# Kernel tuning notes

Hardware: AMD Instinct MI355X
Metric: run time of the kernel (lower is better)

## Reference

```python
import jax, jax.numpy as jnp
import numpy as np

T, B, D, H = 256, 64, 1024, 1024


def setup_inputs() -> dict:
    key = jax.random.key(0)
    ks = jax.random.split(key, 7)
    s = 1.0 / np.sqrt(H)
    return {
        "x": jax.random.normal(ks[0], (T, B, D), dtype=jnp.float32),
        "h0": jax.random.normal(ks[1], (B, H), dtype=jnp.float32),
        "c0": jax.random.normal(ks[2], (B, H), dtype=jnp.float32),
        "W_ih": jax.random.normal(ks[3], (4 * H, D), dtype=jnp.float32) * s,
        "W_hh": jax.random.normal(ks[4], (4 * H, H), dtype=jnp.float32) * s,
        "b_ih": jax.random.normal(ks[5], (4 * H,), dtype=jnp.float32) * s,
        "b_hh": jax.random.normal(ks[6], (4 * H,), dtype=jnp.float32) * s,
    }


def reference(x, h0, c0, W_ih, W_hh, b_ih, b_hh):
    # Reversed-time LSTM: process t = T-1 .. 0, outputs stored in original order.
    def step(carry, xt):
        h, c = carry
        gates = xt @ W_ih.T + b_ih + h @ W_hh.T + b_hh  # [B, 4H]
        i, f, g, o = jnp.split(gates, 4, axis=-1)
        c = jax.nn.sigmoid(f) * c + jax.nn.sigmoid(i) * jnp.tanh(g)
        h = jax.nn.sigmoid(o) * jnp.tanh(c)
        return (h, c), h

    (hT, cT), ys = jax.lax.scan(step, (h0, c0), x, reverse=True)
    return ys, hT, cT
```

## Files before the change

kernel.cpp:

```cpp
#include <hip/hip_runtime.h>
#include <stdint.h>
#include <stddef.h>


typedef unsigned short u16;
typedef __attribute__((ext_vector_type(4))) unsigned short u16x4;
typedef __attribute__((ext_vector_type(8))) short short8;
typedef __attribute__((ext_vector_type(4))) float f32x4;

#define T_LEN 256
#define YS_ELEMS (256 * 64 * 1024)

__device__ __forceinline__ u16 f2bf(float f) {
  union { float f; unsigned int i; } v; v.f = f;
  unsigned int r = v.i + 0x7FFFu + ((v.i >> 16) & 1u);
  return (u16)(r >> 16);
}
__device__ __forceinline__ float bf2f(u16 u) {
  union { unsigned int i; float f; } v; v.i = ((unsigned int)u) << 16; return v.f;
}
__device__ __forceinline__ void gload_lds16(const void* g, void* l) {
  __builtin_amdgcn_global_load_lds(
      (const __attribute__((address_space(1))) unsigned int*)g,
      (__attribute__((address_space(3))) unsigned int*)l, 16, 0, 0);
}
__device__ __forceinline__ float sigm_fast(float x) { return 1.f / (1.f + __expf(-x)); }

#define ISSUE_LD16C(dst, ptr, off)                                      \
  asm volatile("global_load_dwordx4 %0, %1, off offset:%c2"             \
               : "=v"(dst) : "v"(ptr), "i"(off) : "memory")

#define LD8_PLAIN(dst, ptr)                                             \
  asm volatile("global_load_dwordx2 %0, %1, off"                        \
               : "=v"(dst) : "v"(ptr) : "memory")

#define ST8_WT(ptr, val)                                                \
  asm volatile("global_store_dwordx2 %0, %1, off sc0 sc1"               \
               :: "v"(ptr), "v"(val) : "memory")

#define WAIT_VM16() do { asm volatile("s_waitcnt vmcnt(16)" ::: "memory"); \
                         __builtin_amdgcn_sched_barrier(0); } while (0)
#define WAIT_VM0()  do { asm volatile("s_waitcnt vmcnt(0)"  ::: "memory"); \
                         __builtin_amdgcn_sched_barrier(0); } while (0)

__global__ void cast_f32_bf16(const float* __restrict__ src, u16* __restrict__ dst, int n4) {
  int i = blockIdx.x * blockDim.x + threadIdx.x;
  const int stride = gridDim.x * blockDim.x;
  for (; i < n4; i += stride) {
    float4 v = ((const float4*)src)[i];
    u16x4 o;
    o[0] = f2bf(v.x); o[1] = f2bf(v.y); o[2] = f2bf(v.z); o[3] = f2bf(v.w);
    ((u16x4*)dst)[i] = o;
  }
}

__global__ void scat_h0(const float* __restrict__ src, u16* __restrict__ dst) {
  int i = blockIdx.x * blockDim.x + threadIdx.x;
  const int b = i >> 7;
  const int j0 = (i & 127) * 8;
  const float4 v0 = ((const float4*)src)[i * 2];
  const float4 v1 = ((const float4*)src)[i * 2 + 1];
  short8 pk;
  pk[0] = (short)f2bf(v0.x); pk[1] = (short)f2bf(v0.y);
  pk[2] = (short)f2bf(v0.z); pk[3] = (short)f2bf(v0.w);
  pk[4] = (short)f2bf(v1.x); pk[5] = (short)f2bf(v1.y);
  pk[6] = (short)f2bf(v1.z); pk[7] = (short)f2bf(v1.w);
  *(short8*)(dst + (size_t)(j0 >> 4) * 1024 + b * 16 + (j0 & 15)) = pk;
}

__global__ void canary_k(float* __restrict__ out) { out[0] = 100.0f; }

__global__ __launch_bounds__(256, 2) void gemm_pre(
    const u16* __restrict__ X, const u16* __restrict__ Wih,
    const float* __restrict__ bih, const float* __restrict__ bhh,
    u16* __restrict__ Pout)
{
  __shared__ u16 As[128 * 64];
  __shared__ u16 Bs[128 * 64];
  const int tid = threadIdx.x;
  const int lane = tid & 63;
  const int wid = tid >> 6;
  const int wm = wid & 1, wn = wid >> 1;
  const int Mt = blockIdx.x, Nt = blockIdx.y;

  f32x4 acc[4][4] = {};
  const int rsub = lane >> 3;
  const int src_chunk = (lane & 7) ^ rsub;

  for (int it = 0; it < 16; ++it) {
    const int k0 = it * 64;
    #pragma unroll
    for (int q = 0; q < 4; ++q) {
      const int j = wid * 4 + q;
      const int row_local = j * 8 + rsub;
      const u16* ga = X   + ((size_t)(Mt * 128 + row_local)) * 1024 + k0 + src_chunk * 8;
      const u16* gb = Wih + ((size_t)(Nt * 128 + row_local)) * 1024 + k0 + src_chunk * 8;
      gload_lds16(ga, (char*)As + j * 1024);
      gload_lds16(gb, (char*)Bs + j * 1024);
    }
    __syncthreads();
    #pragma unroll
    for (int ks = 0; ks < 2; ++ks) {
      short8 af[4], bfv[4];
      #pragma unroll
      for (int f = 0; f < 4; ++f) {
        const int ra = wm * 64 + f * 16 + (lane & 15);
        const int rb = wn * 64 + f * 16 + (lane & 15);
        const int kc = ks * 4 + (lane >> 4);
        af[f]  = *(const short8*)((const char*)As + ra * 128 + ((kc ^ (ra & 7)) << 4));
        bfv[f] = *(const short8*)((const char*)Bs + rb * 128 + ((kc ^ (rb & 7)) << 4));
      }
      #pragma unroll
      for (int fm = 0; fm < 4; ++fm)
        #pragma unroll
        for (int fn = 0; fn < 4; ++fn)
          acc[fm][fn] = __builtin_amdgcn_mfma_f32_16x16x32_bf16(af[fm], bfv[fn], acc[fm][fn], 0, 0, 0);
    }
    __syncthreads();
  }

  const int t_out = Mt * 2 + wm;
  #pragma unroll
  for (int fn = 0; fn < 4; ++fn) {
    const int n = Nt * 128 + wn * 64 + fn * 16 + (lane & 15);
    const float bias = bih[n] + bhh[n];
    #pragma unroll
    for (int fm = 0; fm < 4; ++fm) {
      const int b = fm * 16 + ((lane >> 4) << 2);
      u16x4 o;
      #pragma unroll
      for (int r = 0; r < 4; ++r) o[r] = f2bf(acc[fm][fn][r] + bias);
      *(u16x4*)(Pout + ((size_t)t_out * 4096 + n) * 64 + b) = o;
    }
  }
}

__global__ __launch_bounds__(256, 1) void lstm_rec(
    const u16* __restrict__ P, const float* __restrict__ c0,
    const float* __restrict__ Whh, u16* __restrict__ ring,
    float* __restrict__ out, int* __restrict__ cnt)
{
  __shared__ u16 Ws[64 * 1024];
  __shared__ float GX[4096];

  const int tid = threadIdx.x;
  const int lane = tid & 63;
  const int wid = tid >> 6;
  const int wg = blockIdx.x;

  {
    const int rowp = tid >> 2;
    const int q = tid & 3;
    const int grow = (rowp >> 4) * 1024 + wg * 16 + (rowp & 15);
    const float4* src = (const float4*)(Whh + (size_t)grow * 1024 + q * 256);
    #pragma unroll 2
    for (int j = 0; j < 32; ++j) {
      float4 v0 = src[j * 2];
      float4 v1 = src[j * 2 + 1];
      short8 pk;
      pk[0] = (short)f2bf(v0.x); pk[1] = (short)f2bf(v0.y);
      pk[2] = (short)f2bf(v0.z); pk[3] = (short)f2bf(v0.w);
      pk[4] = (short)f2bf(v1.x); pk[5] = (short)f2bf(v1.y);
      pk[6] = (short)f2bf(v1.z); pk[7] = (short)f2bf(v1.w);
      const int kc = q * 32 + j;
      *(short8*)((char*)Ws + rowp * 2048 + ((kc ^ (rowp & 7)) << 4)) = pk;
    }
  }

  const int u = tid & 15;
  const int b0 = (tid >> 4) << 2;
  const int jh = wg * 16 + u;
  float cs[4];
  #pragma unroll
  for (int r = 0; r < 4; ++r) cs[r] = c0[(size_t)(b0 + r) * 1024 + jh];

  const int wm = wid & 1;
  const int wn = wid >> 1;
  const int kpos = lane >> 4;

  u16* HXu = (u16*)GX;

  __syncthreads();

  #define ISSUE_Q(buf, qi) {                                                   \
    const u16* bq_ = pA + (size_t)(qi) * 16384;                                \
    _Pragma("unroll")                                                          \
    for (int kq_ = 0; kq_ < 8; ++kq_) {                                        \
      const u16* pk_ = bq_ + kq_ * 2048;                                       \
      ISSUE_LD16C(buf[kq_][0], pk_, 0);                   \
      ISSUE_LD16C(buf[kq_][1], pk_, 512);   \
    } }

  #define MFMA_Q(buf, qi) {                                                    \
    _Pragma("unroll")                                                          \
    for (int kq_ = 0; kq_ < 8; ++kq_) {                                        \
      const int kabs_ = (qi) * 8 + kq_;                                        \
      _Pragma("unroll")                                                        \
      for (int ni_ = 0; ni_ < 2; ++ni_) {                                      \
        const int rs_ = wn * 32 + ni_ * 16 + (lane & 15);                      \
        const int kcl_ = kabs_ * 4 + (lane >> 4);                              \
        const short8 bfr_ = *(const short8*)((const char*)Ws + rs_ * 2048      \
                            + ((kcl_ ^ (rs_ & 7)) << 4));                      \
        acc[0][ni_] = __builtin_amdgcn_mfma_f32_16x16x32_bf16(buf[kq_][0], bfr_, acc[0][ni_], 0, 0, 0); \
        acc[1][ni_] = __builtin_amdgcn_mfma_f32_16x16x32_bf16(buf[kq_][1], bfr_, acc[1][ni_], 0, 0, 0); \
      } } }

  for (int si = 0; si < 256; ++si) {
    const int t = 255 - si;
    const u16* rb = ring + (size_t)si * 65536;

    const u16* pA = rb + (size_t)(kpos >> 1) * 1024 + (kpos & 1) * 8
                    + (wm * 32 + (lane & 15)) * 16;

    const size_t pbase = (size_t)t * 262144;
    unsigned long long Pi, Pf, Pg, Po;
    LD8_PLAIN(Pi, P + pbase + (size_t)(0 * 1024 + jh) * 64 + b0);
    LD8_PLAIN(Pf, P + pbase + (size_t)(1 * 1024 + jh) * 64 + b0);
    LD8_PLAIN(Pg, P + pbase + (size_t)(2 * 1024 + jh) * 64 + b0);
    LD8_PLAIN(Po, P + pbase + (size_t)(3 * 1024 + jh) * 64 + b0);

    f32x4 acc[2][2] = {};
    short8 afrA[8][2], afrB[8][2];

    ISSUE_Q(afrA, 0)
    ISSUE_Q(afrB, 1)
    WAIT_VM16(); MFMA_Q(afrA, 0)
    ISSUE_Q(afrA, 2)
    WAIT_VM16(); MFMA_Q(afrB, 1)
    ISSUE_Q(afrB, 3)
    WAIT_VM16(); MFMA_Q(afrA, 2)
    WAIT_VM0();  MFMA_Q(afrB, 3)

    #pragma unroll
    for (int mi = 0; mi < 2; ++mi)
      #pragma unroll
      for (int ni = 0; ni < 2; ++ni) {
        const int g = wn * 2 + ni;
        const int uu = lane & 15;
        const int bb = wm * 32 + mi * 16 + ((lane >> 4) << 2);
        *(f32x4*)((char*)GX + ((((g * 16 + uu) * 64 + bb) << 2) ^ ((uu & 7) << 4))) = acc[mi][ni];
      }
    __syncthreads();

    const f32x4 vi = *(const f32x4*)((char*)GX + ((((0 * 16 + u) * 64 + b0) << 2) ^ ((u & 7) << 4)));
    const f32x4 vf = *(const f32x4*)((char*)GX + ((((1 * 16 + u) * 64 + b0) << 2) ^ ((u & 7) << 4)));
    const f32x4 vg = *(const f32x4*)((char*)GX + ((((2 * 16 + u) * 64 + b0) << 2) ^ ((u & 7) << 4)));
    const f32x4 vo = *(const f32x4*)((char*)GX + ((((3 * 16 + u) * 64 + b0) << 2) ^ ((u & 7) << 4)));

    float hvv[4], cnn[4];
    #pragma unroll
    for (int r = 0; r < 4; ++r) {
      const float xi = vi[r] + bf2f((u16)(Pi >> (16 * r)));
      const float xf = vf[r] + bf2f((u16)(Pf >> (16 * r)));
      const float xg = vg[r] + bf2f((u16)(Pg >> (16 * r)));
      const float xo = vo[r] + bf2f((u16)(Po >> (16 * r)));
      const float ig = sigm_fast(xi);
      const float fg = sigm_fast(xf);
      const float og = sigm_fast(xo);
      const float cn = fg * cs[r] + ig * tanhf(xg);
      const float hv = og * tanhf(cn);
      cs[r] = cn; cnn[r] = cn; hvv[r] = hv;
    }

    if (si < 255) {
      __syncthreads();
      #pragma unroll
      for (int r = 0; r < 4; ++r) HXu[(b0 + r) * 16 + u] = f2bf(hvv[r]);
      __syncthreads();
      {
        u16* wb = ring + (size_t)(si + 1) * 65536 + (size_t)wg * 1024;
        const unsigned long long hv8 = *(const unsigned long long*)(HXu + tid * 4);
        ST8_WT(wb + tid * 4, hv8);
      }
      WAIT_VM0();
      __syncthreads();
      if (tid == 0) atomicAdd(cnt, 1);
      #pragma unroll
      for (int r = 0; r < 4; ++r)
        out[((size_t)t * 64 + b0 + r) * 1024 + jh] = hvv[r];
      if (tid < 64) {
        while (__hip_atomic_load(cnt, __ATOMIC_RELAXED, __HIP_MEMORY_SCOPE_AGENT)
               < (si + 1) * 64)
          __builtin_amdgcn_s_sleep(2);
      }
      __syncthreads();
    } else {
      #pragma unroll
      for (int r = 0; r < 4; ++r) {
        out[((size_t)t * 64 + b0 + r) * 1024 + jh] = hvv[r];
        out[YS_ELEMS + (size_t)(b0 + r) * 1024 + jh] = hvv[r];
        out[YS_ELEMS + 65536 + (size_t)(b0 + r) * 1024 + jh] = cnn[r];
      }
    }
  }
  #undef ISSUE_Q
  #undef MFMA_Q
}

extern "C" void kernel_launch(void* const* d_in, const int* in_sizes, int n_in,
                              void* d_out, int out_size, void* d_ws, size_t ws_size,
                              hipStream_t stream) {
  const float* x   = (const float*)d_in[0];
  const float* h0  = (const float*)d_in[1];
  const float* c0  = (const float*)d_in[2];
  const float* Wih = (const float*)d_in[3];
  const float* Whh = (const float*)d_in[4];
  const float* bih = (const float*)d_in[5];
  const float* bhh = (const float*)d_in[6];
  float* out = (float*)d_out;

  char* ws = (char*)d_ws;
  u16* x_bf   = (u16*)(ws + 0);
  u16* ring   = (u16*)(ws + 0);
  u16* wih_bf = (u16*)(ws + 33554432);
  u16* Pp     = (u16*)(ws + 41943040);
  int* cnt    = (int*)(ws + 176160768);

  hipLaunchKernelGGL(cast_f32_bf16, dim3(2048), dim3(256), 0, stream, x,   x_bf,   4194304);
  hipLaunchKernelGGL(cast_f32_bf16, dim3(1024), dim3(256), 0, stream, Wih, wih_bf, 1048576);
  hipLaunchKernelGGL(gemm_pre, dim3(128, 32), dim3(256), 0, stream, x_bf, wih_bf, bih, bhh, Pp);
  hipMemsetAsync(cnt, 0, 128, stream);
  hipLaunchKernelGGL(scat_h0, dim3(32), dim3(256), 0, stream, h0, ring);
  hipLaunchKernelGGL(canary_k, dim3(1), dim3(1), 0, stream, out);

  hipLaunchKernelGGL(lstm_rec, dim3(64), dim3(256), 0, stream,
                     (const u16*)Pp, c0, Whh, ring, out, cnt);
}
```

Baseline: 1.812 ms.

## Replace global atomic barrier with per-block sequence flags and per-quarter spin waits

Drops the single atomic counter, where every block waited until all 64 blocks had published. Each block now writes its own step number to a padded flag slot with write-through stores. Before loading each quarter of the hidden state, a block polls only the 16 producer flags for that quarter. This lets the MFMA work for early-ready quarters start before all producers finish. It adds per-step flag polling loads and relies on the ordering of write-through stores for correctness.

```diff
diff --git a/kernel.cpp b/kernel.cpp
--- a/kernel.cpp
+++ b/kernel.cpp
@@ -38,10 +38,24 @@
   asm volatile("global_store_dwordx2 %0, %1, off sc0 sc1"               \
                :: "v"(ptr), "v"(val) : "memory")
 
-#define WAIT_VM16() do { asm volatile("s_waitcnt vmcnt(16)" ::: "memory"); \
+#define ST4_WT(ptr, val)                                                \
+  asm volatile("global_store_dword %0, %1, off sc0 sc1"                 \
+               :: "v"(ptr), "v"(val) : "memory")
+
+#define CHK_ISSUE(dst, qi)                                              \
+  asm volatile("global_load_dword %0, %1, off sc0 sc1"                  \
+               : "=v"(dst) : "v"(seqb + ((((qi) * 16 + flid)) << 5)) : "memory")
+
+#define WAIT_VMN(n) do { asm volatile("s_waitcnt vmcnt(" #n ")" ::: "memory"); \
                          __builtin_amdgcn_sched_barrier(0); } while (0)
-#define WAIT_VM0()  do { asm volatile("s_waitcnt vmcnt(0)"  ::: "memory"); \
-                         __builtin_amdgcn_sched_barrier(0); } while (0)
+
+#define SPIN_Q(fq, qi) do {                                              \
+    while (!__all(fq >= lim)) {                                          \
+      __builtin_amdgcn_s_sleep(1);                                       \
+      CHK_ISSUE(fq, qi);                                                 \
+      WAIT_VMN(0);                                                       \
+    }                                                                    \
+  } while (0)
 
 __global__ void cast_f32_bf16(const float* __restrict__ src, u16* __restrict__ dst, int n4) {
   int i = blockIdx.x * blockDim.x + threadIdx.x;
@@ -138,7 +152,7 @@
 __global__ __launch_bounds__(256, 1) void lstm_rec(
     const u16* __restrict__ P, const float* __restrict__ c0,
     const float* __restrict__ Whh, u16* __restrict__ ring,
-    float* __restrict__ out, int* __restrict__ cnt)
+    float* __restrict__ out, int* __restrict__ seqb)
 {
   __shared__ u16 Ws[64 * 1024];
   __shared__ float GX[4096];
@@ -177,6 +191,7 @@
   const int wm = wid & 1;
   const int wn = wid >> 1;
   const int kpos = lane >> 4;
+  const int flid = lane & 15;
 
   u16* HXu = (u16*)GX;
 
@@ -187,8 +202,8 @@
     _Pragma("unroll")                                                          \
     for (int kq_ = 0; kq_ < 8; ++kq_) {                                        \
       const u16* pk_ = bq_ + kq_ * 2048;                                       \
-      ISSUE_LD16C(buf[kq_][0], pk_, 0);                   \
-      ISSUE_LD16C(buf[kq_][1], pk_, 512);   \
+      ISSUE_LD16C(buf[kq_][0], pk_, 0);                                        \
+      ISSUE_LD16C(buf[kq_][1], pk_, 512);                                      \
     } }
 
   #define MFMA_Q(buf, qi) {                                                    \
@@ -207,29 +222,37 @@
 
   for (int si = 0; si < 256; ++si) {
     const int t = 255 - si;
+    const int lim = si;
     const u16* rb = ring + (size_t)si * 65536;
 
     const u16* pA = rb + (size_t)(kpos >> 1) * 1024 + (kpos & 1) * 8
                     + (wm * 32 + (lane & 15)) * 16;
 
+    int f0, f1, f2, f3;
+    CHK_ISSUE(f0, 0); CHK_ISSUE(f1, 1); CHK_ISSUE(f2, 2); CHK_ISSUE(f3, 3);
     const size_t pbase = (size_t)t * 262144;
     unsigned long long Pi, Pf, Pg, Po;
     LD8_PLAIN(Pi, P + pbase + (size_t)(0 * 1024 + jh) * 64 + b0);
     LD8_PLAIN(Pf, P + pbase + (size_t)(1 * 1024 + jh) * 64 + b0);
     LD8_PLAIN(Pg, P + pbase + (size_t)(2 * 1024 + jh) * 64 + b0);
     LD8_PLAIN(Po, P + pbase + (size_t)(3 * 1024 + jh) * 64 + b0);
+    WAIT_VMN(4);
 
     f32x4 acc[2][2] = {};
     short8 afrA[8][2], afrB[8][2];
 
+    SPIN_Q(f0, 0);
     ISSUE_Q(afrA, 0)
+    SPIN_Q(f1, 1);
     ISSUE_Q(afrB, 1)
-    WAIT_VM16(); MFMA_Q(afrA, 0)
+    WAIT_VMN(16); MFMA_Q(afrA, 0)
+    SPIN_Q(f2, 2);
     ISSUE_Q(afrA, 2)
-    WAIT_VM16(); MFMA_Q(afrB, 1)
+    WAIT_VMN(16); MFMA_Q(afrB, 1)
+    SPIN_Q(f3, 3);
     ISSUE_Q(afrB, 3)
-    WAIT_VM16(); MFMA_Q(afrA, 2)
-    WAIT_VM0();  MFMA_Q(afrB, 3)
+    WAIT_VMN(16); MFMA_Q(afrA, 2)
+    WAIT_VMN(0);  MFMA_Q(afrB, 3)
 
     #pragma unroll
     for (int mi = 0; mi < 2; ++mi)
@@ -272,18 +295,12 @@
         const unsigned long long hv8 = *(const unsigned long long*)(HXu + tid * 4);
         ST8_WT(wb + tid * 4, hv8);
       }
-      WAIT_VM0();
+      WAIT_VMN(0);
       __syncthreads();
-      if (tid == 0) atomicAdd(cnt, 1);
+      if (tid == 0) ST4_WT(seqb + (wg << 5), si + 1);
       #pragma unroll
       for (int r = 0; r < 4; ++r)
         out[((size_t)t * 64 + b0 + r) * 1024 + jh] = hvv[r];
-      if (tid < 64) {
-        while (__hip_atomic_load(cnt, __ATOMIC_RELAXED, __HIP_MEMORY_SCOPE_AGENT)
-               < (si + 1) * 64)
-          __builtin_amdgcn_s_sleep(2);
-      }
-      __syncthreads();
     } else {
       #pragma unroll
       for (int r = 0; r < 4; ++r) {
@@ -314,15 +331,15 @@
   u16* ring   = (u16*)(ws + 0);
   u16* wih_bf = (u16*)(ws + 33554432);
   u16* Pp     = (u16*)(ws + 41943040);
-  int* cnt    = (int*)(ws + 176160768);
+  int* seqb   = (int*)(ws + 176160768);
 
   hipLaunchKernelGGL(cast_f32_bf16, dim3(2048), dim3(256), 0, stream, x,   x_bf,   4194304);
   hipLaunchKernelGGL(cast_f32_bf16, dim3(1024), dim3(256), 0, stream, Wih, wih_bf, 1048576);
   hipLaunchKernelGGL(gemm_pre, dim3(128, 32), dim3(256), 0, stream, x_bf, wih_bf, bih, bhh, Pp);
-  hipMemsetAsync(cnt, 0, 128, stream);
+  hipMemsetAsync(seqb, 0, 8192, stream);
   hipLaunchKernelGGL(scat_h0, dim3(32), dim3(256), 0, stream, h0, ring);
   hipLaunchKernelGGL(canary_k, dim3(1), dim3(1), 0, stream, out);
 
   hipLaunchKernelGGL(lstm_rec, dim3(64), dim3(256), 0, stream,
-                     (const u16*)Pp, c0, Whh, ring, out, cnt);
-}
+                     (const u16*)Pp, c0, Whh, ring, out, seqb);
+}
```

Measured after the change: 1.786 ms. Within noise of the previous version (-1.4%).
